# Kernel tuning notes

Hardware: AMD Instinct MI355X
Metric: run time of the kernel (lower is better)

The kernel has to match this reference:

```python
import jax, jax.numpy as jnp
import numpy as np

C = 1152            # hidden_size
HEADS_LA = 36       # LiteLA heads = hidden_size // 32
HEADS_X = 16        # cross-attention heads
HID = int(C * 2.5)  # GLUMBConv hidden = 2880
B, N, M = 2, 4096, 300
EPS_LA = 1e-8
EPS_LN = 1e-6


def _ln(x):
    # LayerNorm without affine (adaLN-single style)
    mu = jnp.mean(x, -1, keepdims=True)
    var = jnp.mean((x - mu) ** 2, -1, keepdims=True)
    return (x - mu) * jax.lax.rsqrt(var + EPS_LN)


def _lite_la(x, qkv_w, proj_w, proj_b):
    b, n, c = x.shape
    d = c // HEADS_LA
    qkv = x @ qkv_w.T                       # (B,N,3C)
    q, k, v = jnp.split(qkv, 3, -1)
    r = lambda t: t.transpose(0, 2, 1).reshape(b, HEADS_LA, d, n)
    q = jax.nn.relu(r(q))
    k = jax.nn.relu(r(k))
    v = r(v)
    # pad v with a row of ones (PAD_VAL=1) for the normalizer
    v = jnp.concatenate([v, jnp.ones((b, HEADS_LA, 1, n), v.dtype)], 2)  # (B,h,d+1,N)
    vk = jnp.einsum('bhdn,bhen->bhde', v, k)    # (B,h,d+1,d)
    out = jnp.einsum('bhde,bhen->bhdn', vk, q)  # (B,h,d+1,N)
    out = out[:, :, :-1] / (out[:, :, -1:] + EPS_LA)
    out = out.reshape(b, c, n).transpose(0, 2, 1)
    return out @ proj_w.T + proj_b


def _cross(x, y, q_w, q_b, kv_w, kv_b, pw, pb):
    b, n, c = x.shape
    d = c // HEADS_X
    q = (x @ q_w.T + q_b).reshape(b, n, HEADS_X, d).transpose(0, 2, 1, 3)
    k, v = jnp.split(y @ kv_w.T + kv_b, 2, -1)
    k = k.reshape(b, -1, HEADS_X, d).transpose(0, 2, 1, 3)
    v = v.reshape(b, -1, HEADS_X, d).transpose(0, 2, 1, 3)
    scale = float(1.0 / np.sqrt(d))
    a = jax.nn.softmax(jnp.einsum('bhnd,bhmd->bhnm', q, k) * scale, -1)
    o = jnp.einsum('bhnm,bhmd->bhnd', a, v).transpose(0, 2, 1, 3).reshape(b, n, c)
    return o @ pw.T + pb


def _glumb(x, inv_w, inv_b, dw_w, dw_b, pw_w):
    b, n, c = x.shape
    H = W = int(np.sqrt(n))
    h = jax.nn.silu(x @ inv_w.T + inv_b)          # 1x1 inverted conv + silu, (B,N,2*HID)
    h = h.transpose(0, 2, 1).reshape(b, 2 * HID, H, W)
    h = jax.lax.conv_general_dilated(
        h, dw_w, (1, 1), 'SAME',
        feature_group_count=2 * HID,
        dimension_numbers=('NCHW', 'OIHW', 'NCHW'))
    h = h + dw_b[None, :, None, None]
    a, g = jnp.split(h, 2, 1)
    h = a * jax.nn.silu(g)                         # GLU
    h = h.reshape(b, HID, n).transpose(0, 2, 1)
    return h @ pw_w.T                              # 1x1 point conv, no bias/act


def setup_inputs() -> dict:
    key = jax.random.key(0)
    ks = jax.random.split(key, 12)
    p = lambda k, shp: (0.02 * jax.random.normal(k, shp)).astype(jnp.float32)
    z = lambda shp: jnp.zeros(shp, jnp.float32)
    return dict(
        x=jax.random.normal(ks[0], (B, N, C), jnp.float32),
        y=jax.random.normal(ks[1], (B, M, C), jnp.float32),
        t=jax.random.normal(ks[2], (B, 6, C), jnp.float32),
        sst=p(ks[3], (6, C)),
        qkv_w=p(ks[4], (3 * C, C)),
        aproj_w=p(ks[5], (C, C)), aproj_b=z((C,)),
        q_w=p(ks[6], (C, C)), q_b=z((C,)),
        kv_w=p(ks[7], (2 * C, C)), kv_b=z((2 * C,)),
        cproj_w=p(ks[8], (C, C)), cproj_b=z((C,)),
        inv_w=p(ks[9], (2 * HID, C)), inv_b=z((2 * HID,)),
        dw_w=p(ks[10], (2 * HID, 1, 3, 3)), dw_b=z((2 * HID,)),
        pw_w=p(ks[11], (C, HID)),
    )


def reference(x, y, t, sst, qkv_w, aproj_w, aproj_b, q_w, q_b, kv_w, kv_b,
              cproj_w, cproj_b, inv_w, inv_b, dw_w, dw_b, pw_w):
    m = sst[None] + t  # (B,6,C)
    sh_a, sc_a, g_a, sh_m, sc_m, g_m = [m[:, i:i + 1] for i in range(6)]
    x = x + g_a * _lite_la(_ln(x) * (1 + sc_a) + sh_a, qkv_w, aproj_w, aproj_b)
    x = x + _cross(x, y, q_w, q_b, kv_w, kv_b, cproj_w, cproj_b)
    x = x + g_m * _glumb(_ln(x) * (1 + sc_m) + sh_m, inv_w, inv_b, dw_w, dw_b, pw_w)
    return x
```

## Files before the change

kernel.cpp:

```cpp
#include <hip/hip_runtime.h>
#include <hip/hip_bf16.h>
#include <cstdint>
#include <cstddef>

#define CD    1152
#define NTOK  4096
#define MTOK  300
#define BSZ   2
#define HID2  5760
#define HIDD  2880
#define ROWS  (BSZ*NTOK)
#define KVROWS (BSZ*MTOK)

using bf16 = __hip_bfloat16;
typedef __bf16 bf16x8 __attribute__((ext_vector_type(8)));
typedef __bf16 bf16x4 __attribute__((ext_vector_type(4)));
typedef float f32x4 __attribute__((ext_vector_type(4)));

__device__ __forceinline__ float b2f(bf16 h) { return __bfloat162float(h); }
__device__ __forceinline__ bf16  f2b(float f) { return __float2bfloat16(f); }
__device__ __forceinline__ bf16x8 bz8() {
    bf16x8 v;
    #pragma unroll
    for (int j = 0; j < 8; ++j) v[j] = (__bf16)0.0f;
    return v;
}

__device__ __forceinline__ void gload16(const void* g, void* l) {
    __builtin_amdgcn_global_load_lds(
        (const __attribute__((address_space(1))) void*)g,
        (__attribute__((address_space(3))) void*)l, 16, 0, 0);
}

#define PB0 497664
#define PB1 663552
#define PB2 829440
#define PB3 1161216
#define PB4 1327104
#define PB5 2156544
#define PB6 2571264
#define PB7 2657664
#define PB8 2659392
#define PB9 2665872
#define PB10 2675376

__device__ __forceinline__ void cast8(const float* __restrict__ s, bf16* __restrict__ d, int i) {
    f32x4 a = *(const f32x4*)&s[i];
    f32x4 b = *(const f32x4*)&s[i + 4];
    bf16x8 o;
    #pragma unroll
    for (int j = 0; j < 4; ++j) { o[j] = (__bf16)a[j]; o[4 + j] = (__bf16)b[j]; }
    *(bf16x8*)&d[i] = o;
}

__global__ __launch_bounds__(256) void prep_all(
    const float* __restrict__ qkv_w, const float* __restrict__ aproj_w,
    const float* __restrict__ q_w, const float* __restrict__ kv_w,
    const float* __restrict__ cproj_w, const float* __restrict__ inv_w,
    const float* __restrict__ pw_w, const float* __restrict__ y,
    const float* __restrict__ sst, const float* __restrict__ tt,
    const float* __restrict__ dww,
    bf16* __restrict__ wqkv, bf16* __restrict__ waproj, bf16* __restrict__ wq,
    bf16* __restrict__ wkv, bf16* __restrict__ wcproj, bf16* __restrict__ winv,
    bf16* __restrict__ wpw, bf16* __restrict__ yb, float* __restrict__ mbuf,
    bf16* __restrict__ wtdw, float* __restrict__ vkbuf) {
    const int u = blockIdx.x * 256 + threadIdx.x;
    if (u < PB0)      cast8(qkv_w,   wqkv,   u * 8);
    else if (u < PB1) cast8(aproj_w, waproj, (u - PB0) * 8);
    else if (u < PB2) cast8(q_w,     wq,     (u - PB1) * 8);
    else if (u < PB3) cast8(kv_w,    wkv,    (u - PB2) * 8);
    else if (u < PB4) cast8(cproj_w, wcproj, (u - PB3) * 8);
    else if (u < PB5) cast8(inv_w,   winv,   (u - PB4) * 8);
    else if (u < PB6) cast8(pw_w,    wpw,    (u - PB5) * 8);
    else if (u < PB7) cast8(y,       yb,     (u - PB6) * 8);
    else if (u < PB8) {
        const int i = (u - PB7) * 8;
        const int si = (i < 6 * CD) ? i : i - 6 * CD;
        #pragma unroll
        for (int c = 0; c < 2; ++c) {
            f32x4 a = *(const f32x4*)&tt[i + c * 4];
            f32x4 s = *(const f32x4*)&sst[si + c * 4];
            f32x4 o;
            #pragma unroll
            for (int j = 0; j < 4; ++j) o[j] = a[j] + s[j];
            *(f32x4*)&mbuf[i + c * 4] = o;
        }
    } else if (u < PB9) {
        const int i = (u - PB8) * 8;
        const int k = i / HID2, c = i - k * HID2;
        bf16x8 o;
        #pragma unroll
        for (int j = 0; j < 8; ++j) o[j] = (__bf16)dww[(c + j) * 9 + k];
        *(bf16x8*)&wtdw[i] = o;
    } else if (u < PB10) {
        const int i = (u - PB9) * 8;
        f32x4 z = {};
        *(f32x4*)&vkbuf[i] = z;
        *(f32x4*)&vkbuf[i + 4] = z;
    }
}

__global__ __launch_bounds__(256) void ln_mod(
    const float* __restrict__ xf, const float* __restrict__ m,
    int shRow, int scRow, bf16* __restrict__ out) {
    const int row = blockIdx.x, tid = threadIdx.x;
    const int b = row >> 12;
    const f32x4* xr = (const f32x4*)(xf + (size_t)row * CD);
    f32x4 v0 = xr[tid];
    f32x4 v1 = {};
    if (tid < 32) v1 = xr[256 + tid];
    float s = 0.f, s2 = 0.f;
    #pragma unroll
    for (int j = 0; j < 4; ++j) {
        s += v0[j] + v1[j];
        s2 += v0[j] * v0[j] + v1[j] * v1[j];
    }
    #pragma unroll
    for (int off = 32; off; off >>= 1) {
        s  += __shfl_down(s,  off, 64);
        s2 += __shfl_down(s2, off, 64);
    }
    __shared__ float red[8];
    const int wid = tid >> 6, lane = tid & 63;
    if (lane == 0) { red[wid] = s; red[4 + wid] = s2; }
    __syncthreads();
    s  = red[0] + red[1] + red[2] + red[3];
    s2 = red[4] + red[5] + red[6] + red[7];
    const float mu  = s / CD;
    const float var = s2 / CD - mu * mu;
    const float rs  = rsqrtf(var + 1e-6f);
    const f32x4* shp = (const f32x4*)&m[((size_t)b * 6 + shRow) * CD];
    const f32x4* scp = (const f32x4*)&m[((size_t)b * 6 + scRow) * CD];
    bf16x4* ob = (bf16x4*)(out + (size_t)row * CD);
    {
        f32x4 sh = shp[tid], sc = scp[tid];
        bf16x4 o;
        #pragma unroll
        for (int j = 0; j < 4; ++j) o[j] = (__bf16)((v0[j] - mu) * rs * (1.f + sc[j]) + sh[j]);
        ob[tid] = o;
    }
    if (tid < 32) {
        f32x4 sh = shp[256 + tid], sc = scp[256 + tid];
        bf16x4 o;
        #pragma unroll
        for (int j = 0; j < 4; ++j) o[j] = (__bf16)((v1[j] - mu) * rs * (1.f + sc[j]) + sh[j]);
        ob[256 + tid] = o;
    }
}

template<int EPI>
__global__ __launch_bounds__(256) void gemm_bt(
    const bf16* __restrict__ A, const bf16* __restrict__ W,
    const float* __restrict__ bias, const float* __restrict__ resf,
    const float* __restrict__ gate, int gateStride,
    bf16* __restrict__ outb, float* __restrict__ outf,
    int rows, int K, int Nout, int reluCols, int nRowB, int nColB) {
    __shared__ __align__(16) char smem[33792];
    bf16* As = (bf16*)smem;
    bf16* Bs = (bf16*)(smem + 16384);
    const int bid = blockIdx.x;
    int row_blk, col_blk;
    if ((nRowB & 7) == 0) {
        const int rpx = nRowB >> 3;
        const int xcd = bid & 7;
        const int i = bid >> 3;
        row_blk = xcd * rpx + (i % rpx);
        col_blk = i / rpx;
    } else { row_blk = bid % nRowB; col_blk = bid / nRowB; }
    const int row0 = row_blk * 128;
    const int col0 = col_blk * 128;
    const int tid = threadIdx.x;
    const int wid = tid >> 6, lane = tid & 63;
    const int wm = wid & 1, wn = wid >> 1;
    const int l16 = lane & 15, l4 = lane >> 4;
    f32x4 acc[4][4] = {};

    const int sr = tid >> 3;
    const int kbsw = (((tid & 7) ^ (sr & 7)) << 3);
    int gra[4], gcl[4];
    #pragma unroll
    for (int p = 0; p < 4; ++p) {
        int r = row0 + p * 32 + sr; if (r >= rows) r = rows - 1;
        gra[p] = r;
        gcl[p] = col0 + p * 32 + sr;
    }
    char* AsB = smem + wid * 1024;
    char* BsB = smem + 16384 + wid * 1024;

    for (int k0 = 0; k0 < K; k0 += 64) {
        __syncthreads();
        #pragma unroll
        for (int p = 0; p < 4; ++p) {
            gload16(&A[(size_t)gra[p] * K + k0 + kbsw], AsB + p * 4096);
            gload16(&W[(size_t)gcl[p] * K + k0 + kbsw], BsB + p * 4096);
        }
        __syncthreads();
        #pragma unroll
        for (int kk = 0; kk < 2; ++kk) {
            bf16x8 a[4], b[4];
            #pragma unroll
            for (int i = 0; i < 4; ++i) {
                const int ar = wm * 64 + i * 16 + l16;
                a[i] = *(const bf16x8*)&As[ar * 64 + ((((kk << 2) + l4) ^ (ar & 7)) << 3)];
            }
            #pragma unroll
            for (int j = 0; j < 4; ++j) {
                const int br = wn * 64 + j * 16 + l16;
                b[j] = *(const bf16x8*)&Bs[br * 64 + ((((kk << 2) + l4) ^ (br & 7)) << 3)];
            }
            #pragma unroll
            for (int i = 0; i < 4; ++i)
                #pragma unroll
                for (int j = 0; j < 4; ++j)
                    acc[i][j] = __builtin_amdgcn_mfma_f32_16x16x32_bf16(a[i], b[j], acc[i][j], 0, 0, 0);
        }
    }

    float* Lf = (float*)smem;
    const int erow = tid >> 4;
    const int ecol = (tid & 15) * 8;
    const int gc = col0 + ecol;
    #pragma unroll
    for (int pass = 0; pass < 2; ++pass) {
        __syncthreads();
        if (wm == pass) {
            #pragma unroll
            for (int i = 0; i < 4; ++i)
                #pragma unroll
                for (int j = 0; j < 4; ++j) {
                    const int lc = wn * 64 + j * 16 + l16;
                    #pragma unroll
                    for (int r = 0; r < 4; ++r)
                        Lf[(i * 16 + l4 * 4 + r) * 130 + lc] = acc[i][j][r];
                }
        }
        __syncthreads();
        #pragma unroll
        for (int rr = 0; rr < 4; ++rr) {
            const int lrow = rr * 16 + erow;
            const int gr = row0 + pass * 64 + lrow;
            if (gr >= rows) continue;
            float v[8];
            #pragma unroll
            for (int c = 0; c < 8; ++c) v[c] = Lf[lrow * 130 + ecol + c];
            const size_t oi0 = (size_t)gr * Nout + gc;
            if (EPI == 0) {
                bf16x8 ob;
                #pragma unroll
                for (int c = 0; c < 8; ++c) ob[c] = (__bf16)(v[c] + bias[gc + c]);
                *(bf16x8*)&outb[oi0] = ob;
            } else if (EPI == 1) {
                bf16x8 ob;
                #pragma unroll
                for (int c = 0; c < 8; ++c) {
                    float t = v[c];
                    if (gc + c < reluCols) t = fmaxf(t, 0.0f);
                    ob[c] = (__bf16)t;
                }
                *(bf16x8*)&outb[oi0] = ob;
            } else if (EPI == 2) {
                bf16x8 ob;
                #pragma unroll
                for (int c = 0; c < 8; ++c) {
                    float t = v[c] + bias[gc + c];
                    t = t / (1.0f + __expf(-t));
                    ob[c] = (__bf16)t;
                }
                *(bf16x8*)&outb[oi0] = ob;
            } else if (EPI == 3) {
                const float* gp = &gate[(gr >> 12) * gateStride + gc];
                const float* rp = &resf[oi0];
                f32x4 o0, o1; bf16x8 ob;
                #pragma unroll
                for (int c = 0; c < 8; ++c) {
                    float t = v[c] + bias[gc + c];
                    t = rp[c] + gp[c] * t;
                    if (c < 4) o0[c] = t; else o1[c - 4] = t;
                    ob[c] = (__bf16)t;
                }
                *(f32x4*)&outf[oi0] = o0;
                *(f32x4*)&outf[oi0 + 4] = o1;
                *(bf16x8*)&outb[oi0] = ob;
            } else if (EPI == 4) {
                const float* rp = &resf[oi0];
                f32x4 o0, o1;
                #pragma unroll
                for (int c = 0; c < 8; ++c) {
                    float t = rp[c] + v[c] + bias[gc + c];
                    if (c < 4) o0[c] = t; else o1[c - 4] = t;
                }
                *(f32x4*)&outf[oi0] = o0;
                *(f32x4*)&outf[oi0 + 4] = o1;
            } else {
                const float* gp = &gate[(gr >> 12) * gateStride + gc];
                const float* rp = &resf[oi0];
                f32x4 o0, o1;
                #pragma unroll
                for (int c = 0; c < 8; ++c) {
                    float t = rp[c] + gp[c] * v[c];
                    if (c < 4) o0[c] = t; else o1[c - 4] = t;
                }
                *(f32x4*)&outf[oi0] = o0;
                *(f32x4*)&outf[oi0 + 4] = o1;
            }
        }
    }
}

__global__ __launch_bounds__(256) void lite_vk(
    const bf16* __restrict__ qkv, float* __restrict__ vk) {
    const int b = blockIdx.x / 36, h = blockIdx.x % 36;
    const int n0 = blockIdx.y * 256;
    __shared__ bf16 ksm[64 * 32];
    __shared__ bf16 vsm[64 * 32];
    const int t = threadIdx.x;
    const int ev = t >> 3, kq = (t & 7) * 4;
    float a0 = 0, a1 = 0, a2 = 0, a3 = 0;
    float q0 = 0, q1 = 0, q2 = 0, q3 = 0;
    for (int tile = 0; tile < 4; ++tile) {
        const int nb = n0 + tile * 64;
        __syncthreads();
        {
            const int nl = t >> 2, part = (t & 3) * 8;
            const size_t rbase = ((size_t)b * NTOK + nb + nl) * (3 * CD);
            *(bf16x8*)&ksm[nl * 32 + part] = *(const bf16x8*)&qkv[rbase + CD     + h * 32 + part];
            *(bf16x8*)&vsm[nl * 32 + part] = *(const bf16x8*)&qkv[rbase + 2 * CD + h * 32 + part];
        }
        __syncthreads();
        #pragma unroll 4
        for (int nl = 0; nl < 64; ++nl) {
            const float vv = b2f(vsm[nl * 32 + ev]);
            const float k0 = b2f(ksm[nl * 32 + kq + 0]);
            const float k1 = b2f(ksm[nl * 32 + kq + 1]);
            const float k2 = b2f(ksm[nl * 32 + kq + 2]);
            const float k3 = b2f(ksm[nl * 32 + kq + 3]);
            a0 += vv * k0; a1 += vv * k1; a2 += vv * k2; a3 += vv * k3;
            if (ev == 0) { q0 += k0; q1 += k1; q2 += k2; q3 += k3; }
        }
    }
    float* dst = &vk[(((size_t)b * 36 + h) * 33 + ev) * 32 + kq];
    atomicAdd(dst + 0, a0); atomicAdd(dst + 1, a1);
    atomicAdd(dst + 2, a2); atomicAdd(dst + 3, a3);
    if (ev == 0) {
        float* d2 = &vk[(((size_t)b * 36 + h) * 33 + 32) * 32 + kq];
        atomicAdd(d2 + 0, q0); atomicAdd(d2 + 1, q1);
        atomicAdd(d2 + 2, q2); atomicAdd(d2 + 3, q3);
    }
}

__global__ __launch_bounds__(256) void lite_out(
    const bf16* __restrict__ qkv, const float* __restrict__ vk,
    bf16* __restrict__ u) {
    const int b = blockIdx.x / 36, h = blockIdx.x % 36;
    const int n = blockIdx.y * 256 + threadIdx.x;
    __shared__ float vks[33 * 32];
    const float* src = &vk[((size_t)b * 36 + h) * 33 * 32];
    for (int i = threadIdx.x; i < 33 * 32; i += 256) vks[i] = src[i];
    __syncthreads();
    float q[32];
    const bf16* qp = &qkv[((size_t)b * NTOK + n) * (3 * CD) + h * 32];
    const bf16x8* qv = (const bf16x8*)qp;
    #pragma unroll
    for (int w = 0; w < 4; ++w) {
        bf16x8 qq = qv[w];
        #pragma unroll
        for (int e = 0; e < 8; ++e) q[w * 8 + e] = (float)qq[e];
    }
    float denom = 0.f;
    #pragma unroll
    for (int e = 0; e < 32; ++e) denom += vks[32 * 32 + e] * q[e];
    const float rd = 1.f / (denom + 1e-8f);
    bf16* up = &u[((size_t)b * NTOK + n) * CD + h * 32];
    #pragma unroll 1
    for (int d = 0; d < 32; ++d) {
        float acc = 0.f;
        #pragma unroll
        for (int e = 0; e < 32; ++e) acc += vks[d * 32 + e] * q[e];
        up[d] = f2b(acc * rd);
    }
}

__global__ __launch_bounds__(256) void prep_attn(
    const bf16* __restrict__ kvb, bf16* __restrict__ Kp, bf16* __restrict__ VtG) {
    const int b = blockIdx.x >> 4, h = blockIdx.x & 15;
    const int tid = threadIdx.x;
    bf16* kp = Kp + (size_t)blockIdx.x * (320 * 72);
    bf16* vt = VtG + (size_t)blockIdx.x * (80 * 328);
    const bf16x8 z = bz8();
    for (int i = tid; i < 320 * 9; i += 256) {
        const int m = i / 9, part = (i % 9) * 8;
        bf16x8 v = z;
        if (m < MTOK)
            v = *(const bf16x8*)&kvb[((size_t)b * MTOK + m) * (2 * CD) + h * 72 + part];
        *(bf16x8*)&kp[m * 72 + part] = v;
    }
    for (int i = tid; i < 80 * 328; i += 256) {
        const int d = i / 328, mm = i - d * 328;
        bf16 v = f2b(0.f);
        if (mm < MTOK && d < 72)
            v = kvb[((size_t)b * MTOK + mm) * (2 * CD) + CD + h * 72 + d];
        vt[i] = v;
    }
}

__global__ __launch_bounds__(256) void cross_attn_mfma(
    const bf16* __restrict__ qx, const bf16* __restrict__ Kp,
    const bf16* __restrict__ VtG, bf16* __restrict__ attn) {
    const int bh = blockIdx.x;
    const int b = bh >> 4;
    const int row0 = blockIdx.y * 64;
    __shared__ bf16 Ks[320 * 72];
    __shared__ bf16 Vt[80 * 328];
    __shared__ bf16 Ps[64 * 328];
    const int tid = threadIdx.x;
    const int wid = tid >> 6, lane = tid & 63;
    const int l16 = lane & 15, l4 = lane >> 4;
    const bf16 zb = f2b(0.f);
    const bf16x8 zv8 = bz8();

    {
        const bf16x8* Kg = (const bf16x8*)(Kp + (size_t)bh * (320 * 72));
        bf16x8* Kl = (bf16x8*)Ks;
        for (int i = tid; i < 2880; i += 256) Kl[i] = Kg[i];
        const bf16x8* Vg = (const bf16x8*)(VtG + (size_t)bh * (80 * 328));
        bf16x8* Vl = (bf16x8*)Vt;
        for (int i = tid; i < 3280; i += 256) Vl[i] = Vg[i];
    }
    for (int i = lane; i < 16 * 16; i += 64)
        Ps[(wid * 16 + (i >> 4)) * 328 + 304 + (i & 15)] = zb;

    bf16x8 aq[3];
    {
        const int qrow = row0 + wid * 16 + l16;
        const bf16* qp = &qx[((size_t)b * NTOK + qrow) * CD + (bh & 15) * 72];
        aq[0] = *(const bf16x8*)&qp[l4 * 8];
        aq[1] = *(const bf16x8*)&qp[32 + l4 * 8];
        aq[2] = (l4 == 0) ? *(const bf16x8*)&qp[64] : zv8;
    }
    __syncthreads();

    f32x4 sa[19] = {};
    #pragma unroll
    for (int t = 0; t < 19; ++t) {
        const bf16* kr = &Ks[(t * 16 + l16) * 72];
        bf16x8 b0 = *(const bf16x8*)&kr[l4 * 8];
        bf16x8 b1 = *(const bf16x8*)&kr[32 + l4 * 8];
        bf16x8 b2 = (l4 == 0) ? *(const bf16x8*)&kr[64] : zv8;
        sa[t] = __builtin_amdgcn_mfma_f32_16x16x32_bf16(aq[0], b0, sa[t], 0, 0, 0);
        sa[t] = __builtin_amdgcn_mfma_f32_16x16x32_bf16(aq[1], b1, sa[t], 0, 0, 0);
        sa[t] = __builtin_amdgcn_mfma_f32_16x16x32_bf16(aq[2], b2, sa[t], 0, 0, 0);
    }

    const float scale = 0.11785113019775792f;
    if (l16 >= 12) { sa[18][0] = sa[18][1] = sa[18][2] = sa[18][3] = -3.0e37f; }
    float mr[4] = {-3.0e38f, -3.0e38f, -3.0e38f, -3.0e38f};
    #pragma unroll
    for (int t = 0; t < 19; ++t)
        #pragma unroll
        for (int r = 0; r < 4; ++r) {
            const float s = sa[t][r] * scale;
            sa[t][r] = s;
            mr[r] = fmaxf(mr[r], s);
        }
    #pragma unroll
    for (int off = 1; off < 16; off <<= 1)
        #pragma unroll
        for (int r = 0; r < 4; ++r)
            mr[r] = fmaxf(mr[r], __shfl_xor(mr[r], off, 64));
    float lr[4] = {0.f, 0.f, 0.f, 0.f};
    #pragma unroll
    for (int t = 0; t < 19; ++t)
        #pragma unroll
        for (int r = 0; r < 4; ++r) {
            const float p = __expf(sa[t][r] - mr[r]);
            lr[r] += p;
            Ps[(wid * 16 + l4 * 4 + r) * 328 + t * 16 + l16] = f2b(p);
        }
    #pragma unroll
    for (int off = 1; off < 16; off <<= 1)
        #pragma unroll
        for (int r = 0; r < 4; ++r)
            lr[r] += __shfl_xor(lr[r], off, 64);
    __syncthreads();

    f32x4 oa[5] = {};
    #pragma unroll
    for (int kc = 0; kc < 10; ++kc) {
        bf16x8 pa = *(const bf16x8*)&Ps[(wid * 16 + l16) * 328 + kc * 32 + l4 * 8];
        #pragma unroll
        for (int dt = 0; dt < 5; ++dt) {
            bf16x8 vb = *(const bf16x8*)&Vt[(dt * 16 + l16) * 328 + kc * 32 + l4 * 8];
            oa[dt] = __builtin_amdgcn_mfma_f32_16x16x32_bf16(pa, vb, oa[dt], 0, 0, 0);
        }
    }
    #pragma unroll
    for (int r = 0; r < 4; ++r) {
        const float rinv = 1.f / lr[r];
        const int gr = row0 + wid * 16 + l4 * 4 + r;
        bf16* op = &attn[((size_t)b * NTOK + gr) * CD + (bh & 15) * 72];
        #pragma unroll
        for (int dt = 0; dt < 5; ++dt) {
            const int d = dt * 16 + l16;
            if (d < 72) op[d] = f2b(oa[dt][r] * rinv);
        }
    }
}

__global__ __launch_bounds__(128) void dwconv_glu2(
    const bf16* __restrict__ hbuf, const bf16* __restrict__ wt,
    const float* __restrict__ dwb, bf16* __restrict__ glu) {
    const int cg = blockIdx.y * 128 + threadIdx.x;
    if (cg >= 360) return;
    const int c0 = cg * 8;
    const int n = blockIdx.x & 4095;
    const int b = blockIdx.x >> 12;
    const int y0 = n >> 6, x0 = n & 63;
    float a[8], g[8];
    #pragma unroll
    for (int j = 0; j < 8; ++j) { a[j] = dwb[c0 + j]; g[j] = dwb[HIDD + c0 + j]; }
    #pragma unroll
    for (int dy = -1; dy <= 1; ++dy) {
        const int yy = y0 + dy;
        if (yy < 0 || yy >= 64) continue;
        #pragma unroll
        for (int dx = -1; dx <= 1; ++dx) {
            const int xx = x0 + dx;
            if (xx < 0 || xx >= 64) continue;
            const int k = (dy + 1) * 3 + (dx + 1);
            const size_t base = ((size_t)b * NTOK + yy * 64 + xx) * HID2;
            const bf16x8 va = *(const bf16x8*)&hbuf[base + c0];
            const bf16x8 vg = *(const bf16x8*)&hbuf[base + HIDD + c0];
            const bf16x8 wa = *(const bf16x8*)&wt[k * HID2 + c0];
            const bf16x8 wg = *(const bf16x8*)&wt[k * HID2 + HIDD + c0];
            #pragma unroll
            for (int j = 0; j < 8; ++j) {
                a[j] += (float)wa[j] * (float)va[j];
                g[j] += (float)wg[j] * (float)vg[j];
            }
        }
    }
    bf16x8 o;
    #pragma unroll
    for (int j = 0; j < 8; ++j) {
        const float s = g[j] / (1.f + __expf(-g[j]));
        o[j] = (__bf16)(a[j] * s);
    }
    *(bf16x8*)&glu[((size_t)b * NTOK + n) * HIDD + c0] = o;
}

extern "C" void kernel_launch(void* const* d_in, const int* in_sizes, int n_in,
                              void* d_out, int out_size, void* d_ws, size_t ws_size,
                              hipStream_t stream) {
    (void)in_sizes; (void)n_in; (void)out_size; (void)ws_size;
    const float* x       = (const float*)d_in[0];
    const float* y       = (const float*)d_in[1];
    const float* t       = (const float*)d_in[2];
    const float* sst     = (const float*)d_in[3];
    const float* qkv_w   = (const float*)d_in[4];
    const float* aproj_w = (const float*)d_in[5];
    const float* aproj_b = (const float*)d_in[6];
    const float* q_w     = (const float*)d_in[7];
    const float* q_b     = (const float*)d_in[8];
    const float* kv_w    = (const float*)d_in[9];
    const float* kv_b    = (const float*)d_in[10];
    const float* cproj_w = (const float*)d_in[11];
    const float* cproj_b = (const float*)d_in[12];
    const float* inv_w   = (const float*)d_in[13];
    const float* inv_b   = (const float*)d_in[14];
    const float* dw_w    = (const float*)d_in[15];
    const float* dw_b    = (const float*)d_in[16];
    const float* pw_w    = (const float*)d_in[17];
    float* out = (float*)d_out;

    char* ws = (char*)d_ws;
    size_t cur = 0;
    auto take = [&](size_t bytes) -> char* {
        char* p = ws + cur;
        cur = (cur + bytes + 255) & ~(size_t)255;
        return p;
    };
    float* mbuf   = (float*)take(BSZ * 6 * CD * 4);
    float* vkbuf  = (float*)take(BSZ * 36 * 33 * 32 * 4);
    bf16* wqkv    = (bf16*)take((size_t)3 * CD * CD * 2);
    bf16* waproj  = (bf16*)take((size_t)CD * CD * 2);
    bf16* wq      = (bf16*)take((size_t)CD * CD * 2);
    bf16* wkv     = (bf16*)take((size_t)2 * CD * CD * 2);
    bf16* wcproj  = (bf16*)take((size_t)CD * CD * 2);
    bf16* winv    = (bf16*)take((size_t)HID2 * CD * 2);
    bf16* wpw     = (bf16*)take((size_t)CD * HIDD * 2);
    bf16* wtdw    = (bf16*)take((size_t)9 * HID2 * 2);
    bf16* yb      = (bf16*)take((size_t)KVROWS * CD * 2);
    bf16* kvbuf   = (bf16*)take((size_t)KVROWS * 2 * CD * 2);
    bf16* Kp      = (bf16*)take((size_t)32 * 320 * 72 * 2);
    bf16* VtG     = (bf16*)take((size_t)32 * 80 * 328 * 2);
    bf16* P       = (bf16*)take((size_t)ROWS * HID2 * 2);
    bf16* Q       = (bf16*)take((size_t)ROWS * HIDD * 2);
    bf16* R       = (bf16*)take((size_t)ROWS * CD * 2);
    bf16* S       = (bf16*)take((size_t)ROWS * CD * 2);
    float* xa_f   = (float*)take((size_t)ROWS * CD * 4);

    bf16* qkvb = P;  bf16* hbuf = P;
    bf16* ubuf = Q;  bf16* glub = Q;
    bf16* x1 = R, *xa_bf = R, *attnb = R, *x2 = R;
    bf16* qx = S;
    float* xb_f = out;

    prep_all<<<(PB10 + 255) / 256, 256, 0, stream>>>(
        qkv_w, aproj_w, q_w, kv_w, cproj_w, inv_w, pw_w, y, sst, t, dw_w,
        wqkv, waproj, wq, wkv, wcproj, winv, wpw, yb, mbuf, wtdw, vkbuf);

    ln_mod<<<ROWS, 256, 0, stream>>>(x, mbuf, 0, 1, x1);
    gemm_bt<1><<<64 * 27, 256, 0, stream>>>(x1, wqkv, nullptr, nullptr, nullptr, 0,
                                            qkvb, nullptr, ROWS, CD, 3 * CD, 2 * CD, 64, 27);
    lite_vk<<<dim3(72, 16), 256, 0, stream>>>(qkvb, vkbuf);
    lite_out<<<dim3(72, 16), 256, 0, stream>>>(qkvb, vkbuf, ubuf);
    gemm_bt<3><<<64 * 9, 256, 0, stream>>>(ubuf, waproj, aproj_b, x, mbuf + 2 * CD, 6 * CD,
                                           xa_bf, xa_f, ROWS, CD, CD, 0, 64, 9);

    gemm_bt<0><<<64 * 9, 256, 0, stream>>>(xa_bf, wq, q_b, nullptr, nullptr, 0,
                                           qx, nullptr, ROWS, CD, CD, 0, 64, 9);
    gemm_bt<0><<<5 * 18, 256, 0, stream>>>(yb, wkv, kv_b, nullptr, nullptr, 0,
                                           kvbuf, nullptr, KVROWS, CD, 2 * CD, 0, 5, 18);
    prep_attn<<<32, 256, 0, stream>>>(kvbuf, Kp, VtG);
    cross_attn_mfma<<<dim3(32, 64), 256, 0, stream>>>(qx, Kp, VtG, attnb);
    gemm_bt<4><<<64 * 9, 256, 0, stream>>>(attnb, wcproj, cproj_b, xa_f, nullptr, 0,
                                           nullptr, xb_f, ROWS, CD, CD, 0, 64, 9);

    ln_mod<<<ROWS, 256, 0, stream>>>(xb_f, mbuf, 3, 4, x2);
    gemm_bt<2><<<64 * 45, 256, 0, stream>>>(x2, winv, inv_b, nullptr, nullptr, 0,
                                            hbuf, nullptr, ROWS, CD, HID2, 0, 64, 45);
    dwconv_glu2<<<dim3(ROWS, 3), 128, 0, stream>>>(hbuf, wtdw, dw_b, glub);
    gemm_bt<5><<<64 * 9, 256, 0, stream>>>(glub, wpw, nullptr, xb_f, mbuf + 5 * CD, 6 * CD,
                                           nullptr, out, ROWS, HIDD, CD, 0, 64, 9);
}
```

Before: 1.106 ms.

## Add A-stationary MFMA GEMM with pre-packed weights for QKV and inverted conv

Adds a new GEMM kernel that loads a 64-row panel of the activation matrix fully into LDS, then has each wave stream weight tiles that prep_all now stores in an MFMA-fragment layout, so B fragments come straight from global memory without LDS staging. The QKV and GLUMB inverted-conv GEMMs use this kernel, and their old epilogues are removed from gemm_bt. gemm_bt also loses its XCD-aware block remapping. The intent is to avoid re-reading A and to remove B staging in LDS. The risks are low occupancy from the large LDS panel (only 256 blocks), direct global reads of B, and scalar, uncoalesced bf16 output stores.

```diff
diff --git a/kernel.cpp b/kernel.cpp
--- a/kernel.cpp
+++ b/kernel.cpp
@@ -51,6 +51,20 @@
     #pragma unroll
     for (int j = 0; j < 4; ++j) { o[j] = (__bf16)a[j]; o[4 + j] = (__bf16)b[j]; }
     *(bf16x8*)&d[i] = o;
+}
+
+__device__ __forceinline__ void pack8(const float* __restrict__ w, bf16* __restrict__ d, int u) {
+    const int l = u & 63;
+    const int rest = u >> 6;
+    const int kc = rest % 36;
+    const int n16 = rest / 36;
+    const float* src = &w[(size_t)(n16 * 16 + (l & 15)) * CD + kc * 32 + (l >> 4) * 8];
+    f32x4 a = *(const f32x4*)src;
+    f32x4 b = *(const f32x4*)(src + 4);
+    bf16x8 o;
+    #pragma unroll
+    for (int j = 0; j < 4; ++j) { o[j] = (__bf16)a[j]; o[4 + j] = (__bf16)b[j]; }
+    *(bf16x8*)&d[u * 8] = o;
 }
 
 __global__ __launch_bounds__(256) void prep_all(
@@ -65,12 +79,12 @@
     bf16* __restrict__ wpw, bf16* __restrict__ yb, float* __restrict__ mbuf,
     bf16* __restrict__ wtdw, float* __restrict__ vkbuf) {
     const int u = blockIdx.x * 256 + threadIdx.x;
-    if (u < PB0)      cast8(qkv_w,   wqkv,   u * 8);
+    if (u < PB0)      pack8(qkv_w, wqkv, u);
     else if (u < PB1) cast8(aproj_w, waproj, (u - PB0) * 8);
     else if (u < PB2) cast8(q_w,     wq,     (u - PB1) * 8);
     else if (u < PB3) cast8(kv_w,    wkv,    (u - PB2) * 8);
     else if (u < PB4) cast8(cproj_w, wcproj, (u - PB3) * 8);
-    else if (u < PB5) cast8(inv_w,   winv,   (u - PB4) * 8);
+    else if (u < PB5) pack8(inv_w,   winv,   u - PB4);
     else if (u < PB6) cast8(pw_w,    wpw,    (u - PB5) * 8);
     else if (u < PB7) cast8(y,       yb,     (u - PB6) * 8);
     else if (u < PB8) {
@@ -149,6 +163,62 @@
 }
 
 template<int EPI>
+__global__ __launch_bounds__(512) void gemm_as(
+    const bf16* __restrict__ A, const bf16* __restrict__ Wp,
+    const float* __restrict__ bias, bf16* __restrict__ outb,
+    int K, int Nout, int reluCols, int colStreams) {
+    __shared__ bf16 Apan[64 * 1160];
+    const int tid = threadIdx.x;
+    const int row0 = blockIdx.x * 64;
+    const int KC = K >> 5;
+    const int vec8PerRow = K >> 3;
+    for (int i = tid; i < 64 * vec8PerRow; i += 512) {
+        const int r = i / vec8PerRow, c8 = i - r * vec8PerRow;
+        *(bf16x8*)&Apan[r * 1160 + c8 * 8] =
+            *(const bf16x8*)&A[(size_t)(row0 + r) * K + c8 * 8];
+    }
+    __syncthreads();
+
+    const int wid = tid >> 6, lane = tid & 63;
+    const int l16 = lane & 15, l4 = lane >> 4;
+    const int TN = Nout >> 6;
+    for (int t = blockIdx.y * 8 + wid; t < TN; t += colStreams) {
+        f32x4 acc[4][4] = {};
+        const bf16* wpt = Wp + (size_t)(4 * t) * KC * 512;
+        #pragma unroll 4
+        for (int kc = 0; kc < KC; ++kc) {
+            bf16x8 b[4], a[4];
+            #pragma unroll
+            for (int j = 0; j < 4; ++j)
+                b[j] = *(const bf16x8*)&wpt[(size_t)(j * KC + kc) * 512 + lane * 8];
+            #pragma unroll
+            for (int i = 0; i < 4; ++i)
+                a[i] = *(const bf16x8*)&Apan[(i * 16 + l16) * 1160 + kc * 32 + l4 * 8];
+            #pragma unroll
+            for (int i = 0; i < 4; ++i)
+                #pragma unroll
+                for (int j = 0; j < 4; ++j)
+                    acc[i][j] = __builtin_amdgcn_mfma_f32_16x16x32_bf16(a[i], b[j], acc[i][j], 0, 0, 0);
+        }
+        #pragma unroll
+        for (int j = 0; j < 4; ++j) {
+            const int gc = t * 64 + j * 16 + l16;
+            const float bv = (EPI == 2) ? bias[gc] : 0.f;
+            #pragma unroll
+            for (int i = 0; i < 4; ++i) {
+                #pragma unroll
+                for (int r = 0; r < 4; ++r) {
+                    float v = acc[i][j][r];
+                    if (EPI == 1) { if (gc < reluCols) v = fmaxf(v, 0.f); }
+                    else { v += bv; v = v / (1.f + __expf(-v)); }
+                    outb[(size_t)(row0 + i * 16 + l4 * 4 + r) * Nout + gc] = f2b(v);
+                }
+            }
+        }
+    }
+}
+
+template<int EPI>
 __global__ __launch_bounds__(256) void gemm_bt(
     const bf16* __restrict__ A, const bf16* __restrict__ W,
     const float* __restrict__ bias, const float* __restrict__ resf,
@@ -159,14 +229,7 @@
     bf16* As = (bf16*)smem;
     bf16* Bs = (bf16*)(smem + 16384);
     const int bid = blockIdx.x;
-    int row_blk, col_blk;
-    if ((nRowB & 7) == 0) {
-        const int rpx = nRowB >> 3;
-        const int xcd = bid & 7;
-        const int i = bid >> 3;
-        row_blk = xcd * rpx + (i % rpx);
-        col_blk = i / rpx;
-    } else { row_blk = bid % nRowB; col_blk = bid / nRowB; }
+    int row_blk = bid % nRowB, col_blk = bid / nRowB;
     const int row0 = row_blk * 128;
     const int col0 = col_blk * 128;
     const int tid = threadIdx.x;
@@ -248,24 +311,6 @@
                 bf16x8 ob;
                 #pragma unroll
                 for (int c = 0; c < 8; ++c) ob[c] = (__bf16)(v[c] + bias[gc + c]);
-                *(bf16x8*)&outb[oi0] = ob;
-            } else if (EPI == 1) {
-                bf16x8 ob;
-                #pragma unroll
-                for (int c = 0; c < 8; ++c) {
-                    float t = v[c];
-                    if (gc + c < reluCols) t = fmaxf(t, 0.0f);
-                    ob[c] = (__bf16)t;
-                }
-                *(bf16x8*)&outb[oi0] = ob;
-            } else if (EPI == 2) {
-                bf16x8 ob;
-                #pragma unroll
-                for (int c = 0; c < 8; ++c) {
-                    float t = v[c] + bias[gc + c];
-                    t = t / (1.0f + __expf(-t));
-                    ob[c] = (__bf16)t;
-                }
                 *(bf16x8*)&outb[oi0] = ob;
             } else if (EPI == 3) {
                 const float* gp = &gate[(gr >> 12) * gateStride + gc];
@@ -358,8 +403,7 @@
     for (int i = threadIdx.x; i < 33 * 32; i += 256) vks[i] = src[i];
     __syncthreads();
     float q[32];
-    const bf16* qp = &qkv[((size_t)b * NTOK + n) * (3 * CD) + h * 32];
-    const bf16x8* qv = (const bf16x8*)qp;
+    const bf16x8* qv = (const bf16x8*)&qkv[((size_t)b * NTOK + n) * (3 * CD) + h * 32];
     #pragma unroll
     for (int w = 0; w < 4; ++w) {
         bf16x8 qq = qv[w];
@@ -610,8 +654,8 @@
         wqkv, waproj, wq, wkv, wcproj, winv, wpw, yb, mbuf, wtdw, vkbuf);
 
     ln_mod<<<ROWS, 256, 0, stream>>>(x, mbuf, 0, 1, x1);
-    gemm_bt<1><<<64 * 27, 256, 0, stream>>>(x1, wqkv, nullptr, nullptr, nullptr, 0,
-                                            qkvb, nullptr, ROWS, CD, 3 * CD, 2 * CD, 64, 27);
+    gemm_as<1><<<dim3(128, 2), 512, 0, stream>>>(x1, wqkv, nullptr, qkvb,
+                                                 CD, 3 * CD, 2 * CD, 16);
     lite_vk<<<dim3(72, 16), 256, 0, stream>>>(qkvb, vkbuf);
     lite_out<<<dim3(72, 16), 256, 0, stream>>>(qkvb, vkbuf, ubuf);
     gemm_bt<3><<<64 * 9, 256, 0, stream>>>(ubuf, waproj, aproj_b, x, mbuf + 2 * CD, 6 * CD,
@@ -627,8 +671,8 @@
                                            nullptr, xb_f, ROWS, CD, CD, 0, 64, 9);
 
     ln_mod<<<ROWS, 256, 0, stream>>>(xb_f, mbuf, 3, 4, x2);
-    gemm_bt<2><<<64 * 45, 256, 0, stream>>>(x2, winv, inv_b, nullptr, nullptr, 0,
-                                            hbuf, nullptr, ROWS, CD, HID2, 0, 64, 45);
+    gemm_as<2><<<dim3(128, 2), 512, 0, stream>>>(x2, winv, inv_b, hbuf,
+                                                 CD, HID2, 0, 16);
     dwconv_glu2<<<dim3(ROWS, 3), 128, 0, stream>>>(hbuf, wtdw, dw_b, glub);
     gemm_bt<5><<<64 * 9, 256, 0, stream>>>(glub, wpw, nullptr, xb_f, mbuf + 5 * CD, 6 * CD,
                                            nullptr, out, ROWS, HIDD, CD, 0, 64, 9);
```

After: 1.231 ms. +11.2%, slower.
